# Kernel optimization log

Measured on AMD Instinct MI355X. Metric: run time of the kernel, lower is better.

The kernel has to match this reference:

```python
import jax, jax.numpy as jnp
import numpy as np

HEADS = 8
DIM_HEAD = 16          # dim/heads, per default dim_head=None
_DIM = HEADS * DIM_HEAD  # 128
SCALE = DIM_HEAD ** 0.5


def setup_inputs() -> dict:
    key = jax.random.key(0)
    k1, k2, k3 = jax.random.split(key, 3)
    field, batch, dim = 2048, 4, 128
    x = jax.random.normal(k1, (field, batch, dim), dtype=jnp.float32)
    W_qkv = jax.random.normal(k2, (3 * _DIM, dim), dtype=jnp.float32) * (dim ** -0.5)
    W_0 = jax.random.normal(k3, (dim, _DIM), dtype=jnp.float32) * (_DIM ** -0.5)
    b_0 = jnp.zeros((dim,), dtype=jnp.float32)
    return {"x": x, "W_qkv": W_qkv, "W_0": W_0, "b_0": b_0}


def reference(x, W_qkv, W_0, b_0):
    f, b, dim = x.shape
    qkv = x @ W_qkv.T                                  # (f, b, 3*_DIM)
    # reshape (f, b, heads*dim_head) -> (f, b*heads, dim_head), matching torch row-major reshape
    q = qkv[:, :, :_DIM].reshape(f, b * HEADS, DIM_HEAD)
    k = qkv[:, :, _DIM:2 * _DIM].reshape(f, b * HEADS, DIM_HEAD)
    v = qkv[:, :, 2 * _DIM:].reshape(f, b * HEADS, DIM_HEAD)
    # scores over the field axis: (b*heads, f, f)
    scores = jnp.einsum('iqd,jqd->qij', q, k) / SCALE
    attn = jax.nn.softmax(scores, axis=-1)
    out = jnp.einsum('qij,jqd->qid', attn, v)          # (b*heads, f, dim_head)
    out = out.transpose(1, 0, 2)                       # (f, b*heads, dim_head)
    # rearrange 'f (b h) d -> (f b) (h d)'
    out = out.reshape(f, b, HEADS, DIM_HEAD).reshape(f * b, HEADS * DIM_HEAD)
    out = out @ W_0.T + b_0                            # (f*b, dim)
    return out.reshape(f, b, dim)
```

## Files before the change

### kernel.cpp

```cpp
#include <hip/hip_runtime.h>
#include <hip/hip_bf16.h>

#define F_DIM 2048
#define B_DIM 4
#define DIM 128
#define QKV_COLS 384
#define HEADS 8
#define DH 16

#define SHIFT2 14.4269504f
#define QSCALE 0.360673760f

typedef float float4v __attribute__((ext_vector_type(4)));
typedef short short4v __attribute__((ext_vector_type(4)));

static __device__ __forceinline__ unsigned short f2bf(float v) {
    __hip_bfloat16 h = __float2bfloat16(v);
    return __builtin_bit_cast(unsigned short, h);
}
static __device__ __forceinline__ float bf2f(unsigned short u) {
    unsigned int w = ((unsigned int)u) << 16;
    return __builtin_bit_cast(float, w);
}

static __device__ __forceinline__ short4v pack_bf16x4(float a, float b, float c, float d) {
    unsigned plo, phi;
    asm("v_cvt_pk_bf16_f32 %0, %1, %2" : "=v"(plo) : "v"(a), "v"(b));
    asm("v_cvt_pk_bf16_f32 %0, %1, %2" : "=v"(phi) : "v"(c), "v"(d));
    uint2 u{plo, phi};
    return __builtin_bit_cast(short4v, u);
}


__global__ __launch_bounds__(256) void convert_kernel(const float* __restrict__ x,
                                                      const float* __restrict__ Wqkv,
                                                      const float* __restrict__ W0,
                                                      unsigned short* __restrict__ xhi,
                                                      unsigned short* __restrict__ xlo,
                                                      unsigned short* __restrict__ Wbf,
                                                      unsigned short* __restrict__ W0h,
                                                      unsigned short* __restrict__ W0l) {
    if (blockIdx.x < 512) {
        const int tid = blockIdx.x * 256 + threadIdx.x;
        const size_t base = (size_t)tid * 8;
        float v[8];
        *(float4*)(v)     = *(const float4*)(x + base);
        *(float4*)(v + 4) = *(const float4*)(x + base + 4);
        unsigned short h[8], l[8];
#pragma unroll
        for (int j = 0; j < 8; ++j) {
            h[j] = f2bf(v[j]);
            l[j] = f2bf(v[j] - bf2f(h[j]));
        }
        *(uint4*)(xhi + base) = *(const uint4*)h;
        *(uint4*)(xlo + base) = *(const uint4*)l;
    } else if (blockIdx.x < 536) {
        const int t = (blockIdx.x - 512) * 256 + threadIdx.x;
        const size_t base = (size_t)t * 8;
        if (base < (size_t)QKV_COLS * DIM) {
            const int c = (int)(base >> 7);
            const float scale = (c < 128) ? QSCALE : 1.f;
            float v[8];
            *(float4*)(v)     = *(const float4*)(Wqkv + base);
            *(float4*)(v + 4) = *(const float4*)(Wqkv + base + 4);
            unsigned short h[8];
#pragma unroll
            for (int j = 0; j < 8; ++j) h[j] = f2bf(v[j] * scale);
            *(uint4*)(Wbf + base) = *(const uint4*)h;
        }
    } else {
        const int t = (blockIdx.x - 536) * 256 + threadIdx.x;
        const size_t base = (size_t)t * 8;
        if (base < (size_t)DIM * DIM) {
            float v[8];
            *(float4*)(v)     = *(const float4*)(W0 + base);
            *(float4*)(v + 4) = *(const float4*)(W0 + base + 4);
            unsigned short h[8], l[8];
#pragma unroll
            for (int j = 0; j < 8; ++j) {
                h[j] = f2bf(v[j]);
                l[j] = f2bf(v[j] - bf2f(h[j]));
            }
            *(uint4*)(W0h + base) = *(const uint4*)h;
            *(uint4*)(W0l + base) = *(const uint4*)l;
        }
    }
}

__global__ __launch_bounds__(256) void qkv_mfma_kernel(const unsigned short* __restrict__ xhi,
                                                       const unsigned short* __restrict__ xlo,
                                                       const unsigned short* __restrict__ Wbf,
                                                       unsigned short* __restrict__ Qbf,
                                                       unsigned short* __restrict__ Kbf,
                                                       unsigned short* __restrict__ VTt) {
    const int lane = threadIdx.x & 63;
    const int wid = threadIdx.x >> 6;
    const int rbase = blockIdx.x * 64 + wid * 16;
    const int ctbase = blockIdx.y * 6;
    const int lo = lane & 15, hi = lane >> 4;

    const unsigned short* xph = xhi + (size_t)(rbase + lo) * DIM + hi * 4;
    const unsigned short* xpl = xlo + (size_t)(rbase + lo) * DIM + hi * 4;
    short4v xfh[8], xfl[8];
#pragma unroll
    for (int kb = 0; kb < 8; ++kb) {
        xfh[kb] = *(const short4v*)(xph + kb * 16);
        xfl[kb] = *(const short4v*)(xpl + kb * 16);
    }

    float4v d[6];
#pragma unroll
    for (int j = 0; j < 6; ++j) d[j] = (float4v){0.f, 0.f, 0.f, 0.f};

    const unsigned short* wp = Wbf + (size_t)(ctbase * 16 + lo) * DIM + hi * 4;
#pragma unroll
    for (int j = 0; j < 6; ++j) {
#pragma unroll
        for (int kb = 0; kb < 8; ++kb) {
            short4v wf = *(const short4v*)(wp + (size_t)j * 16 * DIM + kb * 16);
            d[j] = __builtin_amdgcn_mfma_f32_16x16x16bf16_1k(wf, xfh[kb], d[j], 0, 0, 0);
            d[j] = __builtin_amdgcn_mfma_f32_16x16x16bf16_1k(wf, xfl[kb], d[j], 0, 0, 0);
        }
    }

    const int i = rbase + lo;
    const int f = i >> 2, bb = i & 3;
#pragma unroll
    for (int j = 0; j < 6; ++j) {
        const int ct = ctbase + j;
        short4v pv = pack_bf16x4(d[j][0], d[j][1], d[j][2], d[j][3]);
        if (ct < 8) {
            unsigned short* dst = Qbf + ((size_t)(bb * 8 + ct) * F_DIM + f) * DH + hi * 4;
            *(uint2*)dst = __builtin_bit_cast(uint2, pv);
        } else if (ct < 16) {
            unsigned short* dst = Kbf + ((size_t)(bb * 8 + (ct - 8)) * F_DIM + f) * DH + hi * 4;
            *(uint2*)dst = __builtin_bit_cast(uint2, pv);
        } else {
            const int hh = ct - 16;
            unsigned short* dst = VTt
                + (((size_t)(bb * 8 + hh) * 128 + (f >> 4)) * 16) * 16 + (f & 15);
#pragma unroll
            for (int r = 0; r < 4; ++r) {
                const int dd = hi * 4 + r;
                dst[(size_t)dd * 16] = (unsigned short)pv[r];
            }
        }
    }
}

__global__ __launch_bounds__(512, 4) void attn_mfma_kernel(const unsigned short* __restrict__ Qbf,
                                                           const unsigned short* __restrict__ Kbf,
                                                           const unsigned short* __restrict__ VTt,
                                                           float* __restrict__ attn) {
    __shared__ float4v comb[2][3][64][5];

    const int bh = blockIdx.y;
    const int b = bh >> 3, h = bh & 7;
    const int lane = threadIdx.x & 63;
    const int wid = threadIdx.x >> 6;
    const int qg = wid & 1;
    const int ch = wid >> 1;
    const int q0 = blockIdx.x * 128 + qg * 64;
    const int lo = lane & 15, hi = lane >> 4;

    const unsigned short* Qp = Qbf + ((size_t)bh * F_DIM + q0 + lo) * DH + hi * 4;
    const short4v qf0 = *(const short4v*)(Qp);
    const short4v qf1 = *(const short4v*)(Qp + 16 * DH);
    const short4v qf2 = *(const short4v*)(Qp + 32 * DH);
    const short4v qf3 = *(const short4v*)(Qp + 48 * DH);

    const unsigned short* Kp = Kbf + (size_t)bh * F_DIM * DH
                             + (size_t)ch * 512 * DH + (size_t)lo * DH + hi * 4;
    const unsigned short* Vp = VTt + ((size_t)bh * 128 + ch * 32) * 256
                             + lo * 16 + hi * 4;

    float4v acc0 = {0.f, 0.f, 0.f, 0.f};
    float4v acc1 = {0.f, 0.f, 0.f, 0.f};
    float4v acc2 = {0.f, 0.f, 0.f, 0.f};
    float4v acc3 = {0.f, 0.f, 0.f, 0.f};
    float4v la0 = {0.f, 0.f, 0.f, 0.f};
    float4v la1 = {0.f, 0.f, 0.f, 0.f};
    float4v la2 = {0.f, 0.f, 0.f, 0.f};
    float4v la3 = {0.f, 0.f, 0.f, 0.f};
    const float4v cinit = {-SHIFT2, -SHIFT2, -SHIFT2, -SHIFT2};

#pragma unroll 2
    for (int kt = 0; kt < 32; ++kt) {
        const short4v kf = *(const short4v*)(Kp + kt * 256);
        const short4v vf = *(const short4v*)(Vp + kt * 256);

        float4v s0 = __builtin_amdgcn_mfma_f32_16x16x16bf16_1k(kf, qf0, cinit, 0, 0, 0);
        float4v s1 = __builtin_amdgcn_mfma_f32_16x16x16bf16_1k(kf, qf1, cinit, 0, 0, 0);
        float4v s2 = __builtin_amdgcn_mfma_f32_16x16x16bf16_1k(kf, qf2, cinit, 0, 0, 0);
        float4v s3 = __builtin_amdgcn_mfma_f32_16x16x16bf16_1k(kf, qf3, cinit, 0, 0, 0);

        float p00 = __builtin_amdgcn_exp2f(s0[0]), p01 = __builtin_amdgcn_exp2f(s0[1]);
        float p02 = __builtin_amdgcn_exp2f(s0[2]), p03 = __builtin_amdgcn_exp2f(s0[3]);
        float p10 = __builtin_amdgcn_exp2f(s1[0]), p11 = __builtin_amdgcn_exp2f(s1[1]);
        float p12 = __builtin_amdgcn_exp2f(s1[2]), p13 = __builtin_amdgcn_exp2f(s1[3]);
        float p20 = __builtin_amdgcn_exp2f(s2[0]), p21 = __builtin_amdgcn_exp2f(s2[1]);
        float p22 = __builtin_amdgcn_exp2f(s2[2]), p23 = __builtin_amdgcn_exp2f(s2[3]);
        float p30 = __builtin_amdgcn_exp2f(s3[0]), p31 = __builtin_amdgcn_exp2f(s3[1]);
        float p32 = __builtin_amdgcn_exp2f(s3[2]), p33 = __builtin_amdgcn_exp2f(s3[3]);

        la0[0] += p00; la0[1] += p01; la0[2] += p02; la0[3] += p03;
        la1[0] += p10; la1[1] += p11; la1[2] += p12; la1[3] += p13;
        la2[0] += p20; la2[1] += p21; la2[2] += p22; la2[3] += p23;
        la3[0] += p30; la3[1] += p31; la3[2] += p32; la3[3] += p33;

        short4v pa0 = pack_bf16x4(p00, p01, p02, p03);
        short4v pa1 = pack_bf16x4(p10, p11, p12, p13);
        short4v pa2 = pack_bf16x4(p20, p21, p22, p23);
        short4v pa3 = pack_bf16x4(p30, p31, p32, p33);

        acc0 = __builtin_amdgcn_mfma_f32_16x16x16bf16_1k(pa0, vf, acc0, 0, 0, 0);
        acc1 = __builtin_amdgcn_mfma_f32_16x16x16bf16_1k(pa1, vf, acc1, 0, 0, 0);
        acc2 = __builtin_amdgcn_mfma_f32_16x16x16bf16_1k(pa2, vf, acc2, 0, 0, 0);
        acc3 = __builtin_amdgcn_mfma_f32_16x16x16bf16_1k(pa3, vf, acc3, 0, 0, 0);
    }

    float l0 = (la0[0] + la0[1]) + (la0[2] + la0[3]);
    float l1 = (la1[0] + la1[1]) + (la1[2] + la1[3]);
    float l2 = (la2[0] + la2[1]) + (la2[2] + la2[3]);
    float l3 = (la3[0] + la3[1]) + (la3[2] + la3[3]);

    if (ch) {
        float4v* pw = comb[qg][ch - 1][lane];
        pw[0] = acc0; pw[1] = acc1; pw[2] = acc2; pw[3] = acc3;
        float4v lv = {l0, l1, l2, l3};
        pw[4] = lv;
    }
    __syncthreads();
    if (!ch) {
#pragma unroll
        for (int part = 0; part < 3; ++part) {
            const float4v* pr = comb[qg][part][lane];
            acc0 += pr[0]; acc1 += pr[1]; acc2 += pr[2]; acc3 += pr[3];
            float4v tl = pr[4];
            l0 += tl[0]; l1 += tl[1]; l2 += tl[2]; l3 += tl[3];
        }

#define STORE_FRAG(ACC, L, FR)                                                  \
        {                                                                       \
            float l = L;                                                        \
            l += __shfl_xor(l, 16);                                             \
            l += __shfl_xor(l, 32);                                             \
            float inv = 1.f / l;                          \
            _Pragma("unroll")                                                   \
            for (int r = 0; r < 4; ++r) {                                       \
                int q = hi * 4 + r;                                             \
                float invq = __shfl(inv, q);                                    \
                int f = q0 + (FR) * 16 + q;                                     \
                attn[((size_t)f * B_DIM + b) * DIM + h * DH + lo] = ACC[r] * invq; \
            }                                                                   \
        }
        STORE_FRAG(acc0, l0, 0)
        STORE_FRAG(acc1, l1, 1)
        STORE_FRAG(acc2, l2, 2)
        STORE_FRAG(acc3, l3, 3)
#undef STORE_FRAG
    }
}

__global__ __launch_bounds__(256) void proj_mfma_kernel(const float* __restrict__ attn,
                                                        const unsigned short* __restrict__ W0h,
                                                        const unsigned short* __restrict__ W0l,
                                                        const float* __restrict__ b0,
                                                        float* __restrict__ out) {
    const int lane = threadIdx.x & 63;
    const int wid = threadIdx.x >> 6;
    const int rbase = blockIdx.x * 64 + wid * 16;
    const int cbase = blockIdx.y * 32;
    const int lo = lane & 15, hi = lane >> 4;

    const float* ap = attn + (size_t)(rbase + lo) * DIM + hi * 4;
    short4v afh[8], afl[8];
#pragma unroll
    for (int kb = 0; kb < 8; ++kb) {
        float4 av = *(const float4*)(ap + kb * 16);
        short4v ah = pack_bf16x4(av.x, av.y, av.z, av.w);
        afh[kb] = ah;
        afl[kb] = pack_bf16x4(av.x - bf2f((unsigned short)ah[0]),
                              av.y - bf2f((unsigned short)ah[1]),
                              av.z - bf2f((unsigned short)ah[2]),
                              av.w - bf2f((unsigned short)ah[3]));
    }

    float4v d[2];
#pragma unroll
    for (int j = 0; j < 2; ++j) d[j] = (float4v){0.f, 0.f, 0.f, 0.f};

    const unsigned short* wph = W0h + (size_t)(cbase + lo) * DIM + hi * 4;
    const unsigned short* wpl = W0l + (size_t)(cbase + lo) * DIM + hi * 4;
#pragma unroll
    for (int j = 0; j < 2; ++j) {
#pragma unroll
        for (int kb = 0; kb < 8; ++kb) {
            short4v wh = *(const short4v*)(wph + (size_t)j * 16 * DIM + kb * 16);
            short4v wl = *(const short4v*)(wpl + (size_t)j * 16 * DIM + kb * 16);
            d[j] = __builtin_amdgcn_mfma_f32_16x16x16bf16_1k(wh, afh[kb], d[j], 0, 0, 0);
            d[j] = __builtin_amdgcn_mfma_f32_16x16x16bf16_1k(wh, afl[kb], d[j], 0, 0, 0);
            d[j] = __builtin_amdgcn_mfma_f32_16x16x16bf16_1k(wl, afh[kb], d[j], 0, 0, 0);
        }
    }

    const int row = rbase + lo;
#pragma unroll
    for (int j = 0; j < 2; ++j) {
        const int col4 = cbase + j * 16 + hi * 4;
        float4 bias = *(const float4*)(b0 + col4);
        float4 o;
        o.x = d[j][0] + bias.x;
        o.y = d[j][1] + bias.y;
        o.z = d[j][2] + bias.z;
        o.w = d[j][3] + bias.w;
        *(float4*)(out + (size_t)row * DIM + col4) = o;
    }
}

extern "C" void kernel_launch(void* const* d_in, const int* in_sizes, int n_in,
                              void* d_out, int out_size, void* d_ws, size_t ws_size,
                              hipStream_t stream) {
    const float* x    = (const float*)d_in[0];
    const float* Wqkv = (const float*)d_in[1];
    const float* W0   = (const float*)d_in[2];
    const float* b0   = (const float*)d_in[3];
    float* out = (float*)d_out;

    char* ws = (char*)d_ws;
    float* attn          = (float*)(ws);
    unsigned short* Qbf  = (unsigned short*)(ws + (4u << 20));
    unsigned short* Kbf  = (unsigned short*)(ws + (6u << 20));
    unsigned short* VTt  = (unsigned short*)(ws + (8u << 20));
    unsigned short* xhi  = (unsigned short*)(ws + (10u << 20));
    unsigned short* xlo  = (unsigned short*)(ws + (12u << 20));
    unsigned short* Wbf  = (unsigned short*)(ws + (14u << 20));
    unsigned short* W0h  = (unsigned short*)(ws + (14u << 20) + (128u << 10));
    unsigned short* W0l  = (unsigned short*)(ws + (14u << 20) + (192u << 10));

    convert_kernel<<<544, 256, 0, stream>>>(x, Wqkv, W0, xhi, xlo, Wbf, W0h, W0l);
    qkv_mfma_kernel<<<dim3(128, 4), 256, 0, stream>>>(xhi, xlo, Wbf, Qbf, Kbf, VTt);
    attn_mfma_kernel<<<dim3(16, 32), 512, 0, stream>>>(Qbf, Kbf, VTt, attn);
    proj_mfma_kernel<<<dim3(128, 4), 256, 0, stream>>>(attn, W0h, W0l, b0, out);
}
```

Before: 62.45 us.

## Fuse x bf16 split into QKV GEMM and widen attention key-split

Removes the separate pass that converts x into hi/lo bf16 buffers; the QKV kernel now reads fp32 x directly and splits it in registers, which saves a full write and re-read of x through global memory. The attention kernel now gives each block one 64-query tile split across 8 waves that each cover 256 keys, instead of two query groups of 4 waves, and it launches twice as many blocks. The partial sums are combined over 7 parts in shared memory. This raises parallelism but lengthens the reduction, and the QKV kernel repeats the conversion for each of its column tiles.

```diff
diff --git a/kernel.cpp b/kernel.cpp
--- a/kernel.cpp
+++ b/kernel.cpp
@@ -32,63 +32,41 @@
 }
 
 
-__global__ __launch_bounds__(256) void convert_kernel(const float* __restrict__ x,
-                                                      const float* __restrict__ Wqkv,
+__global__ __launch_bounds__(256) void convert_kernel(const float* __restrict__ Wqkv,
                                                       const float* __restrict__ W0,
-                                                      unsigned short* __restrict__ xhi,
-                                                      unsigned short* __restrict__ xlo,
                                                       unsigned short* __restrict__ Wbf,
                                                       unsigned short* __restrict__ W0h,
                                                       unsigned short* __restrict__ W0l) {
-    if (blockIdx.x < 512) {
-        const int tid = blockIdx.x * 256 + threadIdx.x;
-        const size_t base = (size_t)tid * 8;
+    if (blockIdx.x < 24) {
+        const int t = blockIdx.x * 256 + threadIdx.x;
+        const size_t base = (size_t)t * 8;
+        const int c = (int)(base >> 7);
+        const float scale = (c < 128) ? QSCALE : 1.f;
         float v[8];
-        *(float4*)(v)     = *(const float4*)(x + base);
-        *(float4*)(v + 4) = *(const float4*)(x + base + 4);
+        *(float4*)(v)     = *(const float4*)(Wqkv + base);
+        *(float4*)(v + 4) = *(const float4*)(Wqkv + base + 4);
+        unsigned short h[8];
+#pragma unroll
+        for (int j = 0; j < 8; ++j) h[j] = f2bf(v[j] * scale);
+        *(uint4*)(Wbf + base) = *(const uint4*)h;
+    } else {
+        const int t = (blockIdx.x - 24) * 256 + threadIdx.x;
+        const size_t base = (size_t)t * 8;
+        float v[8];
+        *(float4*)(v)     = *(const float4*)(W0 + base);
+        *(float4*)(v + 4) = *(const float4*)(W0 + base + 4);
         unsigned short h[8], l[8];
 #pragma unroll
         for (int j = 0; j < 8; ++j) {
             h[j] = f2bf(v[j]);
             l[j] = f2bf(v[j] - bf2f(h[j]));
         }
-        *(uint4*)(xhi + base) = *(const uint4*)h;
-        *(uint4*)(xlo + base) = *(const uint4*)l;
-    } else if (blockIdx.x < 536) {
-        const int t = (blockIdx.x - 512) * 256 + threadIdx.x;
-        const size_t base = (size_t)t * 8;
-        if (base < (size_t)QKV_COLS * DIM) {
-            const int c = (int)(base >> 7);
-            const float scale = (c < 128) ? QSCALE : 1.f;
-            float v[8];
-            *(float4*)(v)     = *(const float4*)(Wqkv + base);
-            *(float4*)(v + 4) = *(const float4*)(Wqkv + base + 4);
-            unsigned short h[8];
-#pragma unroll
-            for (int j = 0; j < 8; ++j) h[j] = f2bf(v[j] * scale);
-            *(uint4*)(Wbf + base) = *(const uint4*)h;
-        }
-    } else {
-        const int t = (blockIdx.x - 536) * 256 + threadIdx.x;
-        const size_t base = (size_t)t * 8;
-        if (base < (size_t)DIM * DIM) {
-            float v[8];
-            *(float4*)(v)     = *(const float4*)(W0 + base);
-            *(float4*)(v + 4) = *(const float4*)(W0 + base + 4);
-            unsigned short h[8], l[8];
-#pragma unroll
-            for (int j = 0; j < 8; ++j) {
-                h[j] = f2bf(v[j]);
-                l[j] = f2bf(v[j] - bf2f(h[j]));
-            }
-            *(uint4*)(W0h + base) = *(const uint4*)h;
-            *(uint4*)(W0l + base) = *(const uint4*)l;
-        }
-    }
-}
-
-__global__ __launch_bounds__(256) void qkv_mfma_kernel(const unsigned short* __restrict__ xhi,
-                                                       const unsigned short* __restrict__ xlo,
+        *(uint4*)(W0h + base) = *(const uint4*)h;
+        *(uint4*)(W0l + base) = *(const uint4*)l;
+    }
+}
+
+__global__ __launch_bounds__(256) void qkv_mfma_kernel(const float* __restrict__ x,
                                                        const unsigned short* __restrict__ Wbf,
                                                        unsigned short* __restrict__ Qbf,
                                                        unsigned short* __restrict__ Kbf,
@@ -99,13 +77,17 @@
     const int ctbase = blockIdx.y * 6;
     const int lo = lane & 15, hi = lane >> 4;
 
-    const unsigned short* xph = xhi + (size_t)(rbase + lo) * DIM + hi * 4;
-    const unsigned short* xpl = xlo + (size_t)(rbase + lo) * DIM + hi * 4;
+    const float* xp = x + (size_t)(rbase + lo) * DIM + hi * 4;
     short4v xfh[8], xfl[8];
 #pragma unroll
     for (int kb = 0; kb < 8; ++kb) {
-        xfh[kb] = *(const short4v*)(xph + kb * 16);
-        xfl[kb] = *(const short4v*)(xpl + kb * 16);
+        float4 xv = *(const float4*)(xp + kb * 16);
+        short4v xh = pack_bf16x4(xv.x, xv.y, xv.z, xv.w);
+        xfh[kb] = xh;
+        xfl[kb] = pack_bf16x4(xv.x - bf2f((unsigned short)xh[0]),
+                              xv.y - bf2f((unsigned short)xh[1]),
+                              xv.z - bf2f((unsigned short)xh[2]),
+                              xv.w - bf2f((unsigned short)xh[3]));
     }
 
     float4v d[6];
@@ -152,15 +134,13 @@
                                                            const unsigned short* __restrict__ Kbf,
                                                            const unsigned short* __restrict__ VTt,
                                                            float* __restrict__ attn) {
-    __shared__ float4v comb[2][3][64][5];
+    __shared__ float4v comb[7][64][5];
 
     const int bh = blockIdx.y;
     const int b = bh >> 3, h = bh & 7;
     const int lane = threadIdx.x & 63;
-    const int wid = threadIdx.x >> 6;
-    const int qg = wid & 1;
-    const int ch = wid >> 1;
-    const int q0 = blockIdx.x * 128 + qg * 64;
+    const int ch = threadIdx.x >> 6;
+    const int q0 = blockIdx.x * 64;
     const int lo = lane & 15, hi = lane >> 4;
 
     const unsigned short* Qp = Qbf + ((size_t)bh * F_DIM + q0 + lo) * DH + hi * 4;
@@ -170,8 +150,8 @@
     const short4v qf3 = *(const short4v*)(Qp + 48 * DH);
 
     const unsigned short* Kp = Kbf + (size_t)bh * F_DIM * DH
-                             + (size_t)ch * 512 * DH + (size_t)lo * DH + hi * 4;
-    const unsigned short* Vp = VTt + ((size_t)bh * 128 + ch * 32) * 256
+                             + (size_t)ch * 256 * DH + (size_t)lo * DH + hi * 4;
+    const unsigned short* Vp = VTt + ((size_t)bh * 128 + ch * 16) * 256
                              + lo * 16 + hi * 4;
 
     float4v acc0 = {0.f, 0.f, 0.f, 0.f};
@@ -185,7 +165,7 @@
     const float4v cinit = {-SHIFT2, -SHIFT2, -SHIFT2, -SHIFT2};
 
 #pragma unroll 2
-    for (int kt = 0; kt < 32; ++kt) {
+    for (int kt = 0; kt < 16; ++kt) {
         const short4v kf = *(const short4v*)(Kp + kt * 256);
         const short4v vf = *(const short4v*)(Vp + kt * 256);
 
@@ -225,7 +205,7 @@
     float l3 = (la3[0] + la3[1]) + (la3[2] + la3[3]);
 
     if (ch) {
-        float4v* pw = comb[qg][ch - 1][lane];
+        float4v* pw = comb[ch - 1][lane];
         pw[0] = acc0; pw[1] = acc1; pw[2] = acc2; pw[3] = acc3;
         float4v lv = {l0, l1, l2, l3};
         pw[4] = lv;
@@ -233,8 +213,8 @@
     __syncthreads();
     if (!ch) {
 #pragma unroll
-        for (int part = 0; part < 3; ++part) {
-            const float4v* pr = comb[qg][part][lane];
+        for (int part = 0; part < 7; ++part) {
+            const float4v* pr = comb[part][lane];
             acc0 += pr[0]; acc1 += pr[1]; acc2 += pr[2]; acc3 += pr[3];
             float4v tl = pr[4];
             l0 += tl[0]; l1 += tl[1]; l2 += tl[2]; l3 += tl[3];
@@ -332,14 +312,12 @@
     unsigned short* Qbf  = (unsigned short*)(ws + (4u << 20));
     unsigned short* Kbf  = (unsigned short*)(ws + (6u << 20));
     unsigned short* VTt  = (unsigned short*)(ws + (8u << 20));
-    unsigned short* xhi  = (unsigned short*)(ws + (10u << 20));
-    unsigned short* xlo  = (unsigned short*)(ws + (12u << 20));
-    unsigned short* Wbf  = (unsigned short*)(ws + (14u << 20));
-    unsigned short* W0h  = (unsigned short*)(ws + (14u << 20) + (128u << 10));
-    unsigned short* W0l  = (unsigned short*)(ws + (14u << 20) + (192u << 10));
-
-    convert_kernel<<<544, 256, 0, stream>>>(x, Wqkv, W0, xhi, xlo, Wbf, W0h, W0l);
-    qkv_mfma_kernel<<<dim3(128, 4), 256, 0, stream>>>(xhi, xlo, Wbf, Qbf, Kbf, VTt);
-    attn_mfma_kernel<<<dim3(16, 32), 512, 0, stream>>>(Qbf, Kbf, VTt, attn);
+    unsigned short* Wbf  = (unsigned short*)(ws + (10u << 20));
+    unsigned short* W0h  = (unsigned short*)(ws + (10u << 20) + (128u << 10));
+    unsigned short* W0l  = (unsigned short*)(ws + (10u << 20) + (192u << 10));
+
+    convert_kernel<<<32, 256, 0, stream>>>(Wqkv, W0, Wbf, W0h, W0l);
+    qkv_mfma_kernel<<<dim3(128, 4), 256, 0, stream>>>(x, Wbf, Qbf, Kbf, VTt);
+    attn_mfma_kernel<<<dim3(32, 32), 512, 0, stream>>>(Qbf, Kbf, VTt, attn);
     proj_mfma_kernel<<<dim3(128, 4), 256, 0, stream>>>(attn, W0h, W0l, b0, out);
 }
```

After: 61.57 us (median of 3 runs). About the same (-1.4%).
